# Kernel optimization log

Hardware: AMD Instinct MI355X
Metric: run time of the kernel (lower is better)

The kernel has to match this reference:

```python
import jax, jax.numpy as jnp
import numpy as np

N_QUBITS = 10
EMBED_DIM = 512
FFN_DIM = 2048
DIM = 2 ** N_QUBITS


def _apply_rx(state, theta, wire):
    # state: (N, 2^n) complex64; theta: scalar or (N,)
    N = state.shape[0]
    hi = 2 ** wire                      # dims before the wire axis (wire 0 = MSB)
    lo = 2 ** (N_QUBITS - 1 - wire)
    s = state.reshape(N, hi, 2, lo)
    th = jnp.asarray(theta, jnp.float32).reshape(-1, 1, 1)  # (N,1,1) or (1,1,1)
    c = jnp.cos(th / 2).astype(jnp.complex64)
    ms = (-1j * jnp.sin(th / 2)).astype(jnp.complex64)
    s0, s1 = s[:, :, 0, :], s[:, :, 1, :]
    out = jnp.stack([c * s0 + ms * s1, ms * s0 + c * s1], axis=2)
    return out.reshape(N, DIM)


def _apply_cnot(state, ctrl, tgt):
    N = state.shape[0]
    s = state.reshape((N,) + (2,) * N_QUBITS)
    s0 = jax.lax.index_in_dim(s, 0, axis=ctrl + 1, keepdims=True)
    s1 = jax.lax.index_in_dim(s, 1, axis=ctrl + 1, keepdims=True)
    s1 = jnp.flip(s1, axis=tgt + 1)  # X on target where control == 1
    return jnp.concatenate([s0, s1], axis=ctrl + 1).reshape(N, DIM)


def _pauliz_signs():
    idx = np.arange(DIM)
    bits = (idx[:, None] >> (N_QUBITS - 1 - np.arange(N_QUBITS))[None, :]) & 1
    return jnp.asarray(1.0 - 2.0 * bits, jnp.float32)  # (2^n, n)


def _quantum_layer(tokens, rx_params):
    # tokens: (N, embed_dim); uses first n_qubits features as encoder angles
    N = tokens.shape[0]
    state = jnp.zeros((N, DIM), jnp.complex64).at[:, 0].set(1.0)
    for w in range(N_QUBITS):                    # encoder: RX(x_w) on wire w
        state = _apply_rx(state, tokens[:, w], w)
    for w in range(N_QUBITS):                    # trainable RX per wire
        state = _apply_rx(state, rx_params[w], w)
    for w in range(N_QUBITS - 1):                # CNOT chain
        state = _apply_cnot(state, w, w + 1)
    state = _apply_cnot(state, N_QUBITS - 1, 0)  # wrap-around CNOT
    probs = state.real ** 2 + state.imag ** 2    # (N, 2^n)
    return probs @ _pauliz_signs()               # (N, n_qubits) <Z_w>


def setup_inputs() -> dict:
    key = jax.random.key(0)
    ks = jax.random.split(key, 6)
    x = jax.random.normal(ks[0], (16, 1024, EMBED_DIM), jnp.float32)
    rx_params = jax.random.normal(ks[1], (N_QUBITS,), jnp.float32)
    lim1 = 1.0 / np.sqrt(N_QUBITS)
    w1 = jax.random.uniform(ks[2], (FFN_DIM, N_QUBITS), jnp.float32, -lim1, lim1)
    b1 = jax.random.uniform(ks[3], (FFN_DIM,), jnp.float32, -lim1, lim1)
    lim2 = 1.0 / np.sqrt(FFN_DIM)
    w2 = jax.random.uniform(ks[4], (EMBED_DIM, FFN_DIM), jnp.float32, -lim2, lim2)
    b2 = jax.random.uniform(ks[5], (EMBED_DIM,), jnp.float32, -lim2, lim2)
    return {"x": x, "rx_params": rx_params, "w1": w1, "b1": b1, "w2": w2, "b2": b2}


def reference(x, rx_params, w1, b1, w2, b2):
    B, S, _ = x.shape
    q_out = _quantum_layer(x.reshape(B * S, EMBED_DIM), rx_params)
    q_out = q_out.reshape(B, S, N_QUBITS)
    h = jax.nn.relu(q_out @ w1.T + b1)           # dropout is identity in eval
    return h @ w2.T + b2
```

## Files before the change

### kernel.cpp

```cpp
#include <hip/hip_runtime.h>
#include <hip/hip_bf16.h>
#include <math.h>


typedef __attribute__((ext_vector_type(8))) short short8;
typedef __attribute__((ext_vector_type(8))) unsigned short ushort8;
typedef __attribute__((ext_vector_type(4))) float fx4;

constexpr int EDIM = 512;
constexpr int FDIM = 2048;
constexpr int NQ   = 10;
constexpr int BK   = 64;
constexpr int NCH  = FDIM / BK;

__device__ __forceinline__ ushort f2bf(float f) {
    union { float f; unsigned u; } v; v.f = f;
    unsigned u = v.u + 0x7FFFu + ((v.u >> 16) & 1u);
    return (ushort)(u >> 16);
}
__device__ __forceinline__ unsigned bits2(__hip_bfloat162 h) {
    union { __hip_bfloat162 h; unsigned u; } v; v.h = h; return v.u;
}
__device__ __forceinline__ void gload_lds16(const void* g, void* l) {
    __builtin_amdgcn_global_load_lds(
        (const __attribute__((address_space(1))) void*)g,
        (__attribute__((address_space(3))) void*)l, 16, 0, 0);
}

__global__ void prep(const float* __restrict__ w2, ushort* __restrict__ w2b) {
    int gid = blockIdx.x * blockDim.x + threadIdx.x;
    int np  = gridDim.x * blockDim.x;
    for (int i = gid; i < EDIM * FDIM / 4; i += np) {
        float4 v = ((const float4*)w2)[i];
        ushort4 o; o.x = f2bf(v.x); o.y = f2bf(v.y); o.z = f2bf(v.z); o.w = f2bf(v.w);
        ((ushort4*)w2b)[i] = o;
    }
}

__global__ __launch_bounds__(256, 2) void gemm1(
    const float* __restrict__ x, const float* __restrict__ rx,
    const float* __restrict__ w1, const float* __restrict__ b1,
    ushort* __restrict__ h, int m_base)
{
    __shared__ float qs[32][NQ];
    const int tid = threadIdx.x;
    const int m0  = m_base + blockIdx.x * 32;

    if (tid < 32) {
        const float* xr = x + (size_t)(m0 + tid) * EDIM;
        float c[NQ], q[NQ];
        #pragma unroll
        for (int w = 0; w < NQ; ++w) c[w] = cosf(xr[w] + rx[w]);
        float p0 = c[1];
        #pragma unroll
        for (int w = 2; w < NQ; ++w) p0 *= c[w];
        q[0] = p0;
        float p = c[0];
        #pragma unroll
        for (int w = 1; w < NQ; ++w) { p *= c[w]; q[w] = p; }
        #pragma unroll
        for (int w = 0; w < NQ; ++w) qs[tid][w] = q[w];
    }
    __syncthreads();

    float wv[80];
    {
        const float4* wp = (const float4*)(w1 + (size_t)tid * 80);
        #pragma unroll
        for (int u = 0; u < 20; ++u) ((float4*)wv)[u] = wp[u];
    }
    float bv[8];
    {
        float4 a = *(const float4*)(b1 + tid * 8);
        float4 b = *(const float4*)(b1 + tid * 8 + 4);
        bv[0]=a.x; bv[1]=a.y; bv[2]=a.z; bv[3]=a.w;
        bv[4]=b.x; bv[5]=b.y; bv[6]=b.z; bv[7]=b.w;
    }
    ushort* hrow = h + (size_t)m0 * FDIM + tid * 8;

    for (int m = 0; m < 32; ++m) {
        float qv[NQ];
        #pragma unroll
        for (int w = 0; w < NQ; ++w) qv[w] = qs[m][w];
        float a[8];
        #pragma unroll
        for (int r = 0; r < 8; ++r) a[r] = bv[r];
        #pragma unroll
        for (int w = 0; w < NQ; ++w)
            #pragma unroll
            for (int r = 0; r < 8; ++r)
                a[r] = fmaf(qv[w], wv[r * 10 + w], a[r]);
        ushort8 o;
        #pragma unroll
        for (int r = 0; r < 4; ++r) {
            unsigned p = bits2(__float22bfloat162_rn(
                make_float2(fmaxf(a[2*r], 0.f), fmaxf(a[2*r+1], 0.f))));
            o[2*r]   = (ushort)(p & 0xFFFFu);
            o[2*r+1] = (ushort)(p >> 16);
        }
        *(ushort8*)(hrow + (size_t)m * FDIM) = o;
    }
}

__global__ __launch_bounds__(256, 2) void gemm2(
    const ushort* __restrict__ h,
    const ushort* __restrict__ w2b,
    const float* __restrict__ b2,
    float* __restrict__ out, int m_base)
{
    __shared__ ushort As[128 * BK];
    __shared__ ushort Bs[128 * BK];

    const int tid  = threadIdx.x;
    const int bm   = blockIdx.x;
    const int bn   = blockIdx.y;
    const int m0   = m_base + bm * 128, n0 = bn * 128;
    const int wave = tid >> 6, lane = tid & 63;
    const int quad = lane >> 4, l16 = lane & 15;
    const int wm   = wave >> 1, wn = wave & 1;

    const int srow0 = tid >> 3;
    const int sbs   = tid & 7;
    const ushort* gA[4]; const ushort* gB[4];
    #pragma unroll
    for (int u = 0; u < 4; ++u) {
        int row = u * 32 + srow0;
        int bl  = sbs ^ (row & 7);
        gA[u] = h   + (size_t)(m0 + row) * FDIM + bl * 8;
        gB[u] = w2b + (size_t)(n0 + row) * FDIM + bl * 8;
    }
    const int ldst = wave * 512;

    const int swz = l16 & 7;
    int aro[4], bro[4];
    #pragma unroll
    for (int t = 0; t < 4; ++t) {
        aro[t] = (wm * 64 + t * 16 + l16) * BK;
        bro[t] = (wn * 64 + t * 16 + l16) * BK;
    }

    fx4 acc[4][4];
    #pragma unroll
    for (int a = 0; a < 4; ++a)
        #pragma unroll
        for (int b = 0; b < 4; ++b) acc[a][b] = fx4{0.f, 0.f, 0.f, 0.f};

    for (int i = 0; i < NCH; ++i) {
        #pragma unroll
        for (int u = 0; u < 4; ++u) {
            gload_lds16(gA[u], &As[u * 2048 + ldst]);
            gload_lds16(gB[u], &Bs[u * 2048 + ldst]);
            gA[u] += BK; gB[u] += BK;
        }
        __syncthreads();

        short8 af[4][2], bf[4][2];
        #pragma unroll
        for (int t = 0; t < 4; ++t)
            #pragma unroll
            for (int hf = 0; hf < 2; ++hf) {
                const int blk = (hf * 4 + quad) ^ swz;
                af[t][hf] = *(const short8*)&As[aro[t] + blk * 8];
                bf[t][hf] = *(const short8*)&Bs[bro[t] + blk * 8];
            }

        #pragma unroll
        for (int hf = 0; hf < 2; ++hf)
            #pragma unroll
            for (int mt = 0; mt < 4; ++mt)
                #pragma unroll
                for (int nt = 0; nt < 4; ++nt)
                    acc[mt][nt] = __builtin_amdgcn_mfma_f32_16x16x32_bf16(
                        af[mt][hf], bf[nt][hf], acc[mt][nt], 0, 0, 0);
        __syncthreads();
    }

    float bb[4];
    #pragma unroll
    for (int nt = 0; nt < 4; ++nt) bb[nt] = b2[n0 + wn * 64 + nt * 16 + l16];
    #pragma unroll
    for (int mt = 0; mt < 4; ++mt) {
        const int mbase = m0 + wm * 64 + mt * 16 + quad * 4;
        #pragma unroll
        for (int nt = 0; nt < 4; ++nt) {
            const int n = n0 + wn * 64 + nt * 16 + l16;
            #pragma unroll
            for (int r = 0; r < 4; ++r)
                out[(size_t)(mbase + r) * EDIM + n] = acc[mt][nt][r] + bb[nt];
        }
    }
}

extern "C" void kernel_launch(void* const* d_in, const int* in_sizes, int n_in,
                              void* d_out, int out_size, void* d_ws, size_t ws_size,
                              hipStream_t stream) {
    const float* x  = (const float*)d_in[0];
    const float* rx = (const float*)d_in[1];
    const float* w1 = (const float*)d_in[2];
    const float* b1 = (const float*)d_in[3];
    const float* w2 = (const float*)d_in[4];
    const float* b2 = (const float*)d_in[5];
    float* out = (float*)d_out;

    const int M = in_sizes[0] / EDIM;

    const size_t w2bytes = (size_t)EDIM * FDIM * 2;
    ushort* w2b = (ushort*)d_ws;
    ushort* h   = (ushort*)((char*)d_ws + w2bytes);

    int Ms = M;
    {
        size_t avail = (ws_size > w2bytes) ? ws_size - w2bytes : 0;
        int cap = (int)(avail / ((size_t)FDIM * 2));
        cap &= ~127;
        if (cap < 128) cap = 128;
        if (Ms > cap) Ms = cap;
    }

    hipLaunchKernelGGL(prep, dim3(256), dim3(256), 0, stream, w2, w2b);

    for (int mb = 0; mb < M; mb += Ms) {
        int cur = (M - mb < Ms) ? (M - mb) : Ms;
        hipLaunchKernelGGL(gemm1, dim3(cur / 32), dim3(256), 0, stream,
                           x, rx, w1, b1, h, mb);
        hipLaunchKernelGGL(gemm2, dim3(cur / 128, 4), dim3(256), 0, stream,
                           h, w2b, b2, out, mb);
    }
}
```

Baseline: 140.4 us.

## Fuse quantum layer, FFN1 and FFN2 into one double-buffered MFMA kernel

Replaces the prep, gemm1 and gemm2 kernels with a single fused kernel. Each block computes the quantum expectations and recomputes its 128x64 slice of the hidden activations on the fly for every K chunk. It also converts fp32 w2 to bf16 in registers while staging it into double-buffered LDS, with a 128x256 tile and 512 threads. This removes the global round-trip of the 16Kx2048 bf16 hidden tensor and the separate weight-conversion pass. In exchange, each block redoes the w1 FMAs (the hidden tile is recomputed by both N-blocks), and the loads move from async global_load_lds to synchronous register-staged stores.

```diff
diff --git a/kernel.cpp b/kernel.cpp
--- a/kernel.cpp
+++ b/kernel.cpp
@@ -4,133 +4,93 @@
 
 
 typedef __attribute__((ext_vector_type(8))) short short8;
-typedef __attribute__((ext_vector_type(8))) unsigned short ushort8;
 typedef __attribute__((ext_vector_type(4))) float fx4;
 
 constexpr int EDIM = 512;
 constexpr int FDIM = 2048;
 constexpr int NQ   = 10;
+constexpr int BM   = 128;
+constexpr int BN   = 256;
 constexpr int BK   = 64;
 constexpr int NCH  = FDIM / BK;
 
-__device__ __forceinline__ ushort f2bf(float f) {
-    union { float f; unsigned u; } v; v.f = f;
-    unsigned u = v.u + 0x7FFFu + ((v.u >> 16) & 1u);
-    return (ushort)(u >> 16);
-}
 __device__ __forceinline__ unsigned bits2(__hip_bfloat162 h) {
     union { __hip_bfloat162 h; unsigned u; } v; v.h = h; return v.u;
 }
-__device__ __forceinline__ void gload_lds16(const void* g, void* l) {
-    __builtin_amdgcn_global_load_lds(
-        (const __attribute__((address_space(1))) void*)g,
-        (__attribute__((address_space(3))) void*)l, 16, 0, 0);
-}
-
-__global__ void prep(const float* __restrict__ w2, ushort* __restrict__ w2b) {
-    int gid = blockIdx.x * blockDim.x + threadIdx.x;
-    int np  = gridDim.x * blockDim.x;
-    for (int i = gid; i < EDIM * FDIM / 4; i += np) {
-        float4 v = ((const float4*)w2)[i];
-        ushort4 o; o.x = f2bf(v.x); o.y = f2bf(v.y); o.z = f2bf(v.z); o.w = f2bf(v.w);
-        ((ushort4*)w2b)[i] = o;
-    }
-}
-
-__global__ __launch_bounds__(256, 2) void gemm1(
+
+__device__ __forceinline__ void hcomp(
+    int k1, int fg, const float* __restrict__ w1, const float* __restrict__ b1,
+    const float* q0, const float* q1, float* hv0, float* hv1)
+{
+    const float* w1p = w1 + (size_t)(k1 + fg * 8) * NQ;
+    float b1v[8];
+    *(float4*)(b1v)     = *(const float4*)(b1 + k1 + fg * 8);
+    *(float4*)(b1v + 4) = *(const float4*)(b1 + k1 + fg * 8 + 4);
+    #pragma unroll
+    for (int g = 0; g < 2; ++g) {
+        float wv[40];
+        #pragma unroll
+        for (int u = 0; u < 10; ++u)
+            ((float4*)wv)[u] = ((const float4*)(w1p + g * 40))[u];
+        #pragma unroll
+        for (int j = 0; j < 4; ++j) {
+            float s0 = b1v[g * 4 + j], s1 = s0;
+            #pragma unroll
+            for (int w = 0; w < NQ; ++w) {
+                s0 = fmaf(q0[w], wv[j * 10 + w], s0);
+                s1 = fmaf(q1[w], wv[j * 10 + w], s1);
+            }
+            hv0[g * 4 + j] = s0; hv1[g * 4 + j] = s1;
+        }
+    }
+}
+
+__global__ __launch_bounds__(512, 2) void fused(
     const float* __restrict__ x, const float* __restrict__ rx,
     const float* __restrict__ w1, const float* __restrict__ b1,
-    ushort* __restrict__ h, int m_base)
+    const float* __restrict__ w2, const float* __restrict__ b2,
+    float* __restrict__ out)
 {
-    __shared__ float qs[32][NQ];
+    __shared__ __align__(16) ushort As[2][BM * BK];
+    __shared__ __align__(16) ushort Bs[2][BN * BK];
+    __shared__ float qs[BM][NQ];
+
     const int tid = threadIdx.x;
-    const int m0  = m_base + blockIdx.x * 32;
-
-    if (tid < 32) {
+    const int m0  = blockIdx.x * BM;
+    const int n0  = blockIdx.y * BN;
+
+    if (tid < BM) {
         const float* xr = x + (size_t)(m0 + tid) * EDIM;
-        float c[NQ], q[NQ];
-        #pragma unroll
-        for (int w = 0; w < NQ; ++w) c[w] = cosf(xr[w] + rx[w]);
+        float4 xa = *(const float4*)xr;
+        float4 xb = *(const float4*)(xr + 4);
+        float2 xc = *(const float2*)(xr + 8);
+        float xv[NQ] = {xa.x, xa.y, xa.z, xa.w, xb.x, xb.y, xb.z, xb.w, xc.x, xc.y};
+        float c[NQ];
+        #pragma unroll
+        for (int w = 0; w < NQ; ++w) c[w] = cosf(xv[w] + rx[w]);
         float p0 = c[1];
         #pragma unroll
         for (int w = 2; w < NQ; ++w) p0 *= c[w];
-        q[0] = p0;
+        qs[tid][0] = p0;
         float p = c[0];
         #pragma unroll
-        for (int w = 1; w < NQ; ++w) { p *= c[w]; q[w] = p; }
-        #pragma unroll
-        for (int w = 0; w < NQ; ++w) qs[tid][w] = q[w];
+        for (int w = 1; w < NQ; ++w) { p *= c[w]; qs[tid][w] = p; }
     }
     __syncthreads();
 
-    float wv[80];
-    {
-        const float4* wp = (const float4*)(w1 + (size_t)tid * 80);
-        #pragma unroll
-        for (int u = 0; u < 20; ++u) ((float4*)wv)[u] = wp[u];
-    }
-    float bv[8];
-    {
-        float4 a = *(const float4*)(b1 + tid * 8);
-        float4 b = *(const float4*)(b1 + tid * 8 + 4);
-        bv[0]=a.x; bv[1]=a.y; bv[2]=a.z; bv[3]=a.w;
-        bv[4]=b.x; bv[5]=b.y; bv[6]=b.z; bv[7]=b.w;
-    }
-    ushort* hrow = h + (size_t)m0 * FDIM + tid * 8;
-
-    for (int m = 0; m < 32; ++m) {
-        float qv[NQ];
-        #pragma unroll
-        for (int w = 0; w < NQ; ++w) qv[w] = qs[m][w];
-        float a[8];
-        #pragma unroll
-        for (int r = 0; r < 8; ++r) a[r] = bv[r];
-        #pragma unroll
-        for (int w = 0; w < NQ; ++w)
-            #pragma unroll
-            for (int r = 0; r < 8; ++r)
-                a[r] = fmaf(qv[w], wv[r * 10 + w], a[r]);
-        ushort8 o;
-        #pragma unroll
-        for (int r = 0; r < 4; ++r) {
-            unsigned p = bits2(__float22bfloat162_rn(
-                make_float2(fmaxf(a[2*r], 0.f), fmaxf(a[2*r+1], 0.f))));
-            o[2*r]   = (ushort)(p & 0xFFFFu);
-            o[2*r+1] = (ushort)(p >> 16);
-        }
-        *(ushort8*)(hrow + (size_t)m * FDIM) = o;
-    }
-}
-
-__global__ __launch_bounds__(256, 2) void gemm2(
-    const ushort* __restrict__ h,
-    const ushort* __restrict__ w2b,
-    const float* __restrict__ b2,
-    float* __restrict__ out, int m_base)
-{
-    __shared__ ushort As[128 * BK];
-    __shared__ ushort Bs[128 * BK];
-
-    const int tid  = threadIdx.x;
-    const int bm   = blockIdx.x;
-    const int bn   = blockIdx.y;
-    const int m0   = m_base + bm * 128, n0 = bn * 128;
+    const int fg = tid & 7;
+    const int mg = tid >> 3;
+    float q0[NQ], q1[NQ];
+    #pragma unroll
+    for (int w = 0; w < NQ; ++w) { q0[w] = qs[2 * mg][w]; q1[w] = qs[2 * mg + 1][w]; }
+
+    const int brow = tid >> 1;
+    const int kh   = tid & 1;
+    const float* w2base = w2 + (size_t)(n0 + brow) * FDIM + kh * 32;
+
     const int wave = tid >> 6, lane = tid & 63;
     const int quad = lane >> 4, l16 = lane & 15;
-    const int wm   = wave >> 1, wn = wave & 1;
-
-    const int srow0 = tid >> 3;
-    const int sbs   = tid & 7;
-    const ushort* gA[4]; const ushort* gB[4];
-    #pragma unroll
-    for (int u = 0; u < 4; ++u) {
-        int row = u * 32 + srow0;
-        int bl  = sbs ^ (row & 7);
-        gA[u] = h   + (size_t)(m0 + row) * FDIM + bl * 8;
-        gB[u] = w2b + (size_t)(n0 + row) * FDIM + bl * 8;
-    }
-    const int ldst = wave * 512;
-
+    const int wm = wave >> 2, wn = wave & 3;
     const int swz = l16 & 7;
     int aro[4], bro[4];
     #pragma unroll
@@ -145,34 +105,114 @@
         #pragma unroll
         for (int b = 0; b < 4; ++b) acc[a][b] = fx4{0.f, 0.f, 0.f, 0.f};
 
-    for (int i = 0; i < NCH; ++i) {
-        #pragma unroll
-        for (int u = 0; u < 4; ++u) {
-            gload_lds16(gA[u], &As[u * 2048 + ldst]);
-            gload_lds16(gB[u], &Bs[u * 2048 + ldst]);
-            gA[u] += BK; gB[u] += BK;
-        }
-        __syncthreads();
-
-        short8 af[4][2], bf[4][2];
-        #pragma unroll
-        for (int t = 0; t < 4; ++t)
-            #pragma unroll
-            for (int hf = 0; hf < 2; ++hf) {
-                const int blk = (hf * 4 + quad) ^ swz;
-                af[t][hf] = *(const short8*)&As[aro[t] + blk * 8];
-                bf[t][hf] = *(const short8*)&Bs[bro[t] + blk * 8];
-            }
-
-        #pragma unroll
-        for (int hf = 0; hf < 2; ++hf)
+    float bqv[32];
+    float hv0[8], hv1[8];
+    #pragma unroll
+    for (int u = 0; u < 8; ++u) ((float4*)bqv)[u] = ((const float4*)w2base)[u];
+    hcomp(0, fg, w1, b1, q0, q1, hv0, hv1);
+    {
+        #pragma unroll
+        for (int g = 0; g < 4; ++g) {
+            short8 o;
+            #pragma unroll
+            for (int p = 0; p < 4; ++p) {
+                unsigned u = bits2(__float22bfloat162_rn(
+                    make_float2(bqv[g * 8 + 2 * p], bqv[g * 8 + 2 * p + 1])));
+                o[2 * p] = (short)(u & 0xFFFFu); o[2 * p + 1] = (short)(u >> 16);
+            }
+            const int blk = (kh * 4 + g) ^ (brow & 7);
+            *(short8*)&Bs[0][brow * BK + blk * 8] = o;
+        }
+        #pragma unroll
+        for (int r2 = 0; r2 < 2; ++r2) {
+            const int row = 2 * mg + r2;
+            const float* hv = r2 ? hv1 : hv0;
+            short8 o;
+            #pragma unroll
+            for (int p = 0; p < 4; ++p) {
+                unsigned u = bits2(__float22bfloat162_rn(
+                    make_float2(fmaxf(hv[2 * p], 0.f), fmaxf(hv[2 * p + 1], 0.f))));
+                o[2 * p] = (short)(u & 0xFFFFu); o[2 * p + 1] = (short)(u >> 16);
+            }
+            const int blk = fg ^ (row & 7);
+            *(short8*)&As[0][row * BK + blk * 8] = o;
+        }
+    }
+    __syncthreads();
+
+    for (int i = 0; i < NCH - 1; ++i) {
+        const int cur = i & 1, nxt = cur ^ 1;
+
+        #pragma unroll
+        for (int u = 0; u < 8; ++u)
+            ((float4*)bqv)[u] = ((const float4*)(w2base + (size_t)(i + 1) * BK))[u];
+
+        #pragma unroll
+        for (int hf = 0; hf < 2; ++hf) {
+            const int blk = ((hf * 4 + quad) ^ swz) * 8;
+            short8 af[4], bfq[4];
+            #pragma unroll
+            for (int t = 0; t < 4; ++t) {
+                af[t]  = *(const short8*)&As[cur][aro[t] + blk];
+                bfq[t] = *(const short8*)&Bs[cur][bro[t] + blk];
+            }
             #pragma unroll
             for (int mt = 0; mt < 4; ++mt)
                 #pragma unroll
                 for (int nt = 0; nt < 4; ++nt)
                     acc[mt][nt] = __builtin_amdgcn_mfma_f32_16x16x32_bf16(
-                        af[mt][hf], bf[nt][hf], acc[mt][nt], 0, 0, 0);
+                        af[mt], bfq[nt], acc[mt][nt], 0, 0, 0);
+        }
+
+        hcomp((i + 1) * BK, fg, w1, b1, q0, q1, hv0, hv1);
+
+        #pragma unroll
+        for (int g = 0; g < 4; ++g) {
+            short8 o;
+            #pragma unroll
+            for (int p = 0; p < 4; ++p) {
+                unsigned u = bits2(__float22bfloat162_rn(
+                    make_float2(bqv[g * 8 + 2 * p], bqv[g * 8 + 2 * p + 1])));
+                o[2 * p] = (short)(u & 0xFFFFu); o[2 * p + 1] = (short)(u >> 16);
+            }
+            const int blk = (kh * 4 + g) ^ (brow & 7);
+            *(short8*)&Bs[nxt][brow * BK + blk * 8] = o;
+        }
+        #pragma unroll
+        for (int r2 = 0; r2 < 2; ++r2) {
+            const int row = 2 * mg + r2;
+            const float* hv = r2 ? hv1 : hv0;
+            short8 o;
+            #pragma unroll
+            for (int p = 0; p < 4; ++p) {
+                unsigned u = bits2(__float22bfloat162_rn(
+                    make_float2(fmaxf(hv[2 * p], 0.f), fmaxf(hv[2 * p + 1], 0.f))));
+                o[2 * p] = (short)(u & 0xFFFFu); o[2 * p + 1] = (short)(u >> 16);
+            }
+            const int blk = fg ^ (row & 7);
+            *(short8*)&As[nxt][row * BK + blk * 8] = o;
+        }
         __syncthreads();
+    }
+
+    {
+        const int cur = (NCH - 1) & 1;
+        #pragma unroll
+        for (int hf = 0; hf < 2; ++hf) {
+            const int blk = ((hf * 4 + quad) ^ swz) * 8;
+            short8 af[4], bfq[4];
+            #pragma unroll
+            for (int t = 0; t < 4; ++t) {
+                af[t]  = *(const short8*)&As[cur][aro[t] + blk];
+                bfq[t] = *(const short8*)&Bs[cur][bro[t] + blk];
+            }
+            #pragma unroll
+            for (int mt = 0; mt < 4; ++mt)
+                #pragma unroll
+                for (int nt = 0; nt < 4; ++nt)
+                    acc[mt][nt] = __builtin_amdgcn_mfma_f32_16x16x32_bf16(
+                        af[mt], bfq[nt], acc[mt][nt], 0, 0, 0);
+        }
     }
 
     float bb[4];
@@ -200,30 +240,11 @@
     const float* b1 = (const float*)d_in[3];
     const float* w2 = (const float*)d_in[4];
     const float* b2 = (const float*)d_in[5];
-    float* out = (float*)d_out;
 
     const int M = in_sizes[0] / EDIM;
 
-    const size_t w2bytes = (size_t)EDIM * FDIM * 2;
-    ushort* w2b = (ushort*)d_ws;
-    ushort* h   = (ushort*)((char*)d_ws + w2bytes);
-
-    int Ms = M;
-    {
-        size_t avail = (ws_size > w2bytes) ? ws_size - w2bytes : 0;
-        int cap = (int)(avail / ((size_t)FDIM * 2));
-        cap &= ~127;
-        if (cap < 128) cap = 128;
-        if (Ms > cap) Ms = cap;
-    }
-
-    hipLaunchKernelGGL(prep, dim3(256), dim3(256), 0, stream, w2, w2b);
-
-    for (int mb = 0; mb < M; mb += Ms) {
-        int cur = (M - mb < Ms) ? (M - mb) : Ms;
-        hipLaunchKernelGGL(gemm1, dim3(cur / 32), dim3(256), 0, stream,
-                           x, rx, w1, b1, h, mb);
-        hipLaunchKernelGGL(gemm2, dim3(cur / 128, 4), dim3(256), 0, stream,
-                           h, w2b, b2, out, mb);
-    }
-}
+    (void)d_ws; (void)ws_size; (void)n_in; (void)out_size;
+
+    hipLaunchKernelGGL(fused, dim3(M / BM, EDIM / BN), dim3(512), 0, stream,
+                       x, rx, w1, b1, w2, b2, (float*)d_out);
+}
```

New measurement: 240.7 us. 71.4% more time.

## Double-buffer gemm2 LDS tiles with 256x128 blocks and interleaved MFMA phases

Applied to the files above, without the earlier changes.

Rewrites the second GEMM to use 512-thread blocks with 256x128 output tiles and double-buffered LDS. Global-to-LDS loads for the next K tile are issued between MFMA quadrant phases, using explicit vmcnt waits, barriers and setprio to overlap memory with compute. This replaces the load-sync-compute-sync loop that exposed load latency each iteration. It increases LDS use to 96KB per block, which limits occupancy, and relies on hand-placed waitcnts being correct.

```diff
diff --git a/kernel.cpp b/kernel.cpp
--- a/kernel.cpp
+++ b/kernel.cpp
@@ -11,7 +11,11 @@
 constexpr int FDIM = 2048;
 constexpr int NQ   = 10;
 constexpr int BK   = 64;
-constexpr int NCH  = FDIM / BK;
+constexpr int BM2  = 256;
+constexpr int BN2  = 128;
+constexpr int NT2  = FDIM / BK;
+constexpr int ABUF = BM2 * BK;
+constexpr int BBUF = BN2 * BK;
 
 __device__ __forceinline__ ushort f2bf(float f) {
     union { float f; unsigned u; } v; v.f = f;
@@ -26,6 +30,12 @@
         (const __attribute__((address_space(1))) void*)g,
         (__attribute__((address_space(3))) void*)l, 16, 0, 0);
 }
+
+#define SBAR()   __builtin_amdgcn_s_barrier()
+#define LGKM0()  asm volatile("s_waitcnt lgkmcnt(0)" ::: "memory")
+#define SCHED0() __builtin_amdgcn_sched_barrier(0)
+#define VMCNT6() asm volatile("s_waitcnt vmcnt(6)" ::: "memory")
+#define VMCNT0() asm volatile("s_waitcnt vmcnt(0)" ::: "memory")
 
 __global__ void prep(const float* __restrict__ w2, ushort* __restrict__ w2b) {
     int gid = blockIdx.x * blockDim.x + threadIdx.x;
@@ -102,36 +112,33 @@
     }
 }
 
-__global__ __launch_bounds__(256, 2) void gemm2(
+__global__ __launch_bounds__(512, 2) void gemm2(
     const ushort* __restrict__ h,
     const ushort* __restrict__ w2b,
     const float* __restrict__ b2,
     float* __restrict__ out, int m_base)
 {
-    __shared__ ushort As[128 * BK];
-    __shared__ ushort Bs[128 * BK];
+    __shared__ __align__(16) ushort As[2 * ABUF];
+    __shared__ __align__(16) ushort Bs[2 * BBUF];
 
     const int tid  = threadIdx.x;
-    const int bm   = blockIdx.x;
-    const int bn   = blockIdx.y;
-    const int m0   = m_base + bm * 128, n0 = bn * 128;
+    const int m0   = m_base + blockIdx.x * BM2;
+    const int n0   = blockIdx.y * BN2;
     const int wave = tid >> 6, lane = tid & 63;
     const int quad = lane >> 4, l16 = lane & 15;
     const int wm   = wave >> 1, wn = wave & 1;
-
-    const int srow0 = tid >> 3;
-    const int sbs   = tid & 7;
-    const ushort* gA[4]; const ushort* gB[4];
-    #pragma unroll
-    for (int u = 0; u < 4; ++u) {
-        int row = u * 32 + srow0;
-        int bl  = sbs ^ (row & 7);
-        gA[u] = h   + (size_t)(m0 + row) * FDIM + bl * 8;
-        gB[u] = w2b + (size_t)(n0 + row) * FDIM + bl * 8;
-    }
-    const int ldst = wave * 512;
-
-    const int swz = l16 & 7;
+    const int swz  = l16 & 7;
+
+    const int srow = tid >> 3;
+    const int bl   = (tid & 7) ^ (srow & 7);
+    const ushort* pA[4]; const ushort* pB[2];
+    #pragma unroll
+    for (int u = 0; u < 4; ++u)
+        pA[u] = h + (size_t)(m0 + u * 64 + srow) * FDIM + bl * 8;
+    #pragma unroll
+    for (int u = 0; u < 2; ++u)
+        pB[u] = w2b + (size_t)(n0 + u * 64 + srow) * FDIM + bl * 8;
+
     int aro[4], bro[4];
     #pragma unroll
     for (int t = 0; t < 4; ++t) {
@@ -145,35 +152,79 @@
         #pragma unroll
         for (int b = 0; b < 4; ++b) acc[a][b] = fx4{0.f, 0.f, 0.f, 0.f};
 
-    for (int i = 0; i < NCH; ++i) {
-        #pragma unroll
-        for (int u = 0; u < 4; ++u) {
-            gload_lds16(gA[u], &As[u * 2048 + ldst]);
-            gload_lds16(gB[u], &Bs[u * 2048 + ldst]);
-            gA[u] += BK; gB[u] += BK;
-        }
-        __syncthreads();
-
-        short8 af[4][2], bf[4][2];
-        #pragma unroll
-        for (int t = 0; t < 4; ++t)
-            #pragma unroll
-            for (int hf = 0; hf < 2; ++hf) {
-                const int blk = (hf * 4 + quad) ^ swz;
-                af[t][hf] = *(const short8*)&As[aro[t] + blk * 8];
-                bf[t][hf] = *(const short8*)&Bs[bro[t] + blk * 8];
-            }
-
-        #pragma unroll
-        for (int hf = 0; hf < 2; ++hf)
-            #pragma unroll
-            for (int mt = 0; mt < 4; ++mt)
-                #pragma unroll
-                for (int nt = 0; nt < 4; ++nt)
-                    acc[mt][nt] = __builtin_amdgcn_mfma_f32_16x16x32_bf16(
-                        af[mt][hf], bf[nt][hf], acc[mt][nt], 0, 0, 0);
-        __syncthreads();
-    }
+#define RDA(Ab, PAIR, fr) do { \
+    _Pragma("unroll") for (int m_ = 0; m_ < 2; ++m_) \
+    _Pragma("unroll") for (int hf = 0; hf < 2; ++hf) \
+        fr[m_][hf] = *(const short8*)&(Ab)[aro[(PAIR)*2+m_] + (((hf*4+quad)^swz)<<3)]; \
+} while(0)
+#define RDB(Bb, PAIR, fr) do { \
+    _Pragma("unroll") for (int n_ = 0; n_ < 2; ++n_) \
+    _Pragma("unroll") for (int hf = 0; hf < 2; ++hf) \
+        fr[n_][hf] = *(const short8*)&(Bb)[bro[(PAIR)*2+n_] + (((hf*4+quad)^swz)<<3)]; \
+} while(0)
+#define MMQ(Af, Bf, MO, NO) do { \
+    _Pragma("unroll") for (int hf = 0; hf < 2; ++hf) \
+    _Pragma("unroll") for (int m_ = 0; m_ < 2; ++m_) \
+    _Pragma("unroll") for (int n_ = 0; n_ < 2; ++n_) \
+        acc[(MO)+m_][(NO)+n_] = __builtin_amdgcn_mfma_f32_16x16x32_bf16( \
+            Af[m_][hf], Bf[n_][hf], acc[(MO)+m_][(NO)+n_], 0, 0, 0); \
+} while(0)
+
+    #pragma unroll
+    for (int u = 0; u < 4; ++u) { gload_lds16(pA[u], As + u * 4096 + wave * 512); pA[u] += BK; }
+    #pragma unroll
+    for (int u = 0; u < 2; ++u) { gload_lds16(pB[u], Bs + u * 4096 + wave * 512); pB[u] += BK; }
+    #pragma unroll
+    for (int u = 0; u < 4; ++u) { gload_lds16(pA[u], As + ABUF + u * 4096 + wave * 512); pA[u] += BK; }
+    #pragma unroll
+    for (int u = 0; u < 2; ++u) { gload_lds16(pB[u], Bs + BBUF + u * 4096 + wave * 512); pB[u] += BK; }
+    VMCNT6();
+    SBAR();
+
+#define KTILE(T, MODE) do { \
+    const ushort* Ab = As + ((T) & 1) * ABUF; \
+    const ushort* Bb = Bs + ((T) & 1) * BBUF; \
+    ushort* Aw = As + ((T) & 1) * ABUF; \
+    ushort* Bw = Bs + ((T) & 1) * BBUF; \
+    short8 a0[2][2], a1[2][2], b0[2][2], b1[2][2]; \
+     \
+    RDA(Ab, 0, a0); RDB(Bb, 0, b0); \
+    SBAR(); LGKM0(); SCHED0(); \
+    __builtin_amdgcn_s_setprio(1); MMQ(a0, b0, 0, 0); __builtin_amdgcn_s_setprio(0); \
+    SBAR(); \
+     \
+    RDB(Bb, 1, b1); \
+    SBAR(); LGKM0(); SCHED0(); \
+    __builtin_amdgcn_s_setprio(1); MMQ(a0, b1, 0, 2); __builtin_amdgcn_s_setprio(0); \
+    SBAR(); \
+     \
+    RDA(Ab, 1, a1); \
+    if ((MODE) == 0) { \
+        _Pragma("unroll") for (int u = 0; u < 2; ++u) { \
+            gload_lds16(pB[u], Bw + u * 4096 + wave * 512); pB[u] += BK; } \
+    } \
+    SBAR(); LGKM0(); SCHED0(); \
+    __builtin_amdgcn_s_setprio(1); MMQ(a1, b1, 2, 2); __builtin_amdgcn_s_setprio(0); \
+    SBAR(); \
+     \
+    if ((MODE) == 0) { \
+        _Pragma("unroll") for (int u = 0; u < 4; ++u) { \
+            gload_lds16(pA[u], Aw + u * 4096 + wave * 512); pA[u] += BK; } \
+        VMCNT6(); \
+    } else if ((MODE) == 1) { VMCNT0(); } \
+    SBAR(); \
+    __builtin_amdgcn_s_setprio(1); MMQ(a1, b0, 2, 0); __builtin_amdgcn_s_setprio(0); \
+    SBAR(); \
+} while(0)
+
+    for (int t = 0; t < NT2 - 2; ++t) KTILE(t, 0);
+    KTILE(NT2 - 2, 1);
+    KTILE(NT2 - 1, 2);
+
+#undef KTILE
+#undef MMQ
+#undef RDA
+#undef RDB
 
     float bb[4];
     #pragma unroll
@@ -212,8 +263,8 @@
     {
         size_t avail = (ws_size > w2bytes) ? ws_size - w2bytes : 0;
         int cap = (int)(avail / ((size_t)FDIM * 2));
-        cap &= ~127;
-        if (cap < 128) cap = 128;
+        cap &= ~255;
+        if (cap < 256) cap = 256;
         if (Ms > cap) Ms = cap;
     }
 
@@ -223,7 +274,7 @@
         int cur = (M - mb < Ms) ? (M - mb) : Ms;
         hipLaunchKernelGGL(gemm1, dim3(cur / 32), dim3(256), 0, stream,
                            x, rx, w1, b1, h, mb);
-        hipLaunchKernelGGL(gemm2, dim3(cur / 128, 4), dim3(256), 0, stream,
+        hipLaunchKernelGGL(gemm2, dim3(cur / BM2, EDIM / BN2), dim3(512), 0, stream,
                            h, w2b, b2, out, mb);
     }
 }
```

Result: slower. 146.9 us (+4.6%).

## Triple-buffer gemm2 LDS loads and enlarge tile to 256x128 with 8 waves

Applied to the files above, without the earlier changes.

Rewrites the second GEMM main loop as a three-stage software pipeline. Async global-to-LDS loads for a future K chunk are issued before computing on the current chunk, and only vmcnt-counted waits plus a single barrier are used per iteration. The block tile grows to 256x128 with 512 threads, which improves reuse of the B operand. MFMA sections are wrapped in raised wave priority. The cost is about 147KB of LDS per block, which allows only one block per CU, and the grid is halved to 256 blocks.

```diff
diff --git a/kernel.cpp b/kernel.cpp
--- a/kernel.cpp
+++ b/kernel.cpp
@@ -11,7 +11,11 @@
 constexpr int FDIM = 2048;
 constexpr int NQ   = 10;
 constexpr int BK   = 64;
-constexpr int NCH  = FDIM / BK;
+constexpr int BM2  = 256;
+constexpr int BN2  = 128;
+constexpr int NT2  = FDIM / BK;
+constexpr int ABUF = BM2 * BK;
+constexpr int BBUF = BN2 * BK;
 
 __device__ __forceinline__ ushort f2bf(float f) {
     union { float f; unsigned u; } v; v.f = f;
@@ -26,6 +30,11 @@
         (const __attribute__((address_space(1))) void*)g,
         (__attribute__((address_space(3))) void*)l, 16, 0, 0);
 }
+
+#define SBAR()   __builtin_amdgcn_s_barrier()
+#define FENCE()  asm volatile("" ::: "memory")
+#define VMCNT6() asm volatile("s_waitcnt vmcnt(6)" ::: "memory")
+#define VMCNT0() asm volatile("s_waitcnt vmcnt(0)" ::: "memory")
 
 __global__ void prep(const float* __restrict__ w2, ushort* __restrict__ w2b) {
     int gid = blockIdx.x * blockDim.x + threadIdx.x;
@@ -102,36 +111,33 @@
     }
 }
 
-__global__ __launch_bounds__(256, 2) void gemm2(
+__global__ __launch_bounds__(512, 2) void gemm2(
     const ushort* __restrict__ h,
     const ushort* __restrict__ w2b,
     const float* __restrict__ b2,
     float* __restrict__ out, int m_base)
 {
-    __shared__ ushort As[128 * BK];
-    __shared__ ushort Bs[128 * BK];
+    __shared__ __align__(16) ushort As[3 * ABUF];
+    __shared__ __align__(16) ushort Bs[3 * BBUF];
 
     const int tid  = threadIdx.x;
-    const int bm   = blockIdx.x;
-    const int bn   = blockIdx.y;
-    const int m0   = m_base + bm * 128, n0 = bn * 128;
+    const int m0   = m_base + blockIdx.x * BM2;
+    const int n0   = blockIdx.y * BN2;
     const int wave = tid >> 6, lane = tid & 63;
     const int quad = lane >> 4, l16 = lane & 15;
     const int wm   = wave >> 1, wn = wave & 1;
-
-    const int srow0 = tid >> 3;
-    const int sbs   = tid & 7;
-    const ushort* gA[4]; const ushort* gB[4];
-    #pragma unroll
-    for (int u = 0; u < 4; ++u) {
-        int row = u * 32 + srow0;
-        int bl  = sbs ^ (row & 7);
-        gA[u] = h   + (size_t)(m0 + row) * FDIM + bl * 8;
-        gB[u] = w2b + (size_t)(n0 + row) * FDIM + bl * 8;
-    }
-    const int ldst = wave * 512;
-
-    const int swz = l16 & 7;
+    const int swz  = l16 & 7;
+
+    const int srow = tid >> 3;
+    const int bl   = (tid & 7) ^ (srow & 7);
+    const ushort* pA[4]; const ushort* pB[2];
+    #pragma unroll
+    for (int u = 0; u < 4; ++u)
+        pA[u] = h + (size_t)(m0 + u * 64 + srow) * FDIM + bl * 8;
+    #pragma unroll
+    for (int u = 0; u < 2; ++u)
+        pB[u] = w2b + (size_t)(n0 + u * 64 + srow) * FDIM + bl * 8;
+
     int aro[4], bro[4];
     #pragma unroll
     for (int t = 0; t < 4; ++t) {
@@ -145,35 +151,70 @@
         #pragma unroll
         for (int b = 0; b < 4; ++b) acc[a][b] = fx4{0.f, 0.f, 0.f, 0.f};
 
-    for (int i = 0; i < NCH; ++i) {
-        #pragma unroll
-        for (int u = 0; u < 4; ++u) {
-            gload_lds16(gA[u], &As[u * 2048 + ldst]);
-            gload_lds16(gB[u], &Bs[u * 2048 + ldst]);
-            gA[u] += BK; gB[u] += BK;
-        }
-        __syncthreads();
-
+#define STAGE_A(dst) do { _Pragma("unroll") \
+    for (int u = 0; u < 4; ++u) { gload_lds16(pA[u], (dst) + u * 4096 + wave * 512); pA[u] += BK; } } while(0)
+#define STAGE_B(dst) do { _Pragma("unroll") \
+    for (int u = 0; u < 2; ++u) { gload_lds16(pB[u], (dst) + u * 4096 + wave * 512); pB[u] += BK; } } while(0)
+#define RDFRAGS(Ab, Bb, af, bf) do { _Pragma("unroll") \
+    for (int t = 0; t < 4; ++t) _Pragma("unroll") \
+    for (int hf = 0; hf < 2; ++hf) { \
+        const int blk = (((hf * 4 + quad) ^ swz) << 3); \
+        af[t][hf] = *(const short8*)&(Ab)[aro[t] + blk]; \
+        bf[t][hf] = *(const short8*)&(Bb)[bro[t] + blk]; \
+    } } while(0)
+#define MMALL(af, bf) do { _Pragma("unroll") \
+    for (int hf = 0; hf < 2; ++hf) _Pragma("unroll") \
+    for (int mt = 0; mt < 4; ++mt) _Pragma("unroll") \
+    for (int nt = 0; nt < 4; ++nt) \
+        acc[mt][nt] = __builtin_amdgcn_mfma_f32_16x16x32_bf16( \
+            af[mt][hf], bf[nt][hf], acc[mt][nt], 0, 0, 0); } while(0)
+
+    STAGE_A(As); STAGE_B(Bs);
+    STAGE_A(As + ABUF); STAGE_B(Bs + BBUF);
+    VMCNT6();
+    SBAR(); FENCE();
+
+    int cur = 0, stg = 2;
+    for (int t = 0; t < NT2 - 2; ++t) {
+        ushort* Aw = As + stg * ABUF;
+        ushort* Bw = Bs + stg * BBUF;
+        STAGE_A(Aw); STAGE_B(Bw);
+
+        const ushort* Ab = As + cur * ABUF;
+        const ushort* Bb = Bs + cur * BBUF;
         short8 af[4][2], bf[4][2];
-        #pragma unroll
-        for (int t = 0; t < 4; ++t)
-            #pragma unroll
-            for (int hf = 0; hf < 2; ++hf) {
-                const int blk = (hf * 4 + quad) ^ swz;
-                af[t][hf] = *(const short8*)&As[aro[t] + blk * 8];
-                bf[t][hf] = *(const short8*)&Bs[bro[t] + blk * 8];
-            }
-
-        #pragma unroll
-        for (int hf = 0; hf < 2; ++hf)
-            #pragma unroll
-            for (int mt = 0; mt < 4; ++mt)
-                #pragma unroll
-                for (int nt = 0; nt < 4; ++nt)
-                    acc[mt][nt] = __builtin_amdgcn_mfma_f32_16x16x32_bf16(
-                        af[mt][hf], bf[nt][hf], acc[mt][nt], 0, 0, 0);
-        __syncthreads();
-    }
+        RDFRAGS(Ab, Bb, af, bf);
+        __builtin_amdgcn_s_setprio(1);
+        MMALL(af, bf);
+        __builtin_amdgcn_s_setprio(0);
+
+        VMCNT6();
+        SBAR(); FENCE();
+        cur = (cur == 2) ? 0 : cur + 1;
+        stg = (stg == 2) ? 0 : stg + 1;
+    }
+
+    {
+        short8 af[4][2], bf[4][2];
+        RDFRAGS(As, Bs, af, bf);
+        __builtin_amdgcn_s_setprio(1);
+        MMALL(af, bf);
+        __builtin_amdgcn_s_setprio(0);
+        VMCNT0();
+        SBAR(); FENCE();
+    }
+    {
+        short8 af[4][2], bf[4][2];
+        RDFRAGS(As + ABUF, Bs + BBUF, af, bf);
+        __builtin_amdgcn_s_setprio(1);
+        MMALL(af, bf);
+        __builtin_amdgcn_s_setprio(0);
+    }
+
+#undef MMALL
+#undef RDFRAGS
+#undef STAGE_A
+#undef STAGE_B
 
     float bb[4];
     #pragma unroll
@@ -212,8 +253,8 @@
     {
         size_t avail = (ws_size > w2bytes) ? ws_size - w2bytes : 0;
         int cap = (int)(avail / ((size_t)FDIM * 2));
-        cap &= ~127;
-        if (cap < 128) cap = 128;
+        cap &= ~255;
+        if (cap < 256) cap = 256;
         if (Ms > cap) Ms = cap;
     }
 
@@ -223,7 +264,7 @@
         int cur = (M - mb < Ms) ? (M - mb) : Ms;
         hipLaunchKernelGGL(gemm1, dim3(cur / 32), dim3(256), 0, stream,
                            x, rx, w1, b1, h, mb);
-        hipLaunchKernelGGL(gemm2, dim3(cur / 128, 4), dim3(256), 0, stream,
+        hipLaunchKernelGGL(gemm2, dim3(cur / BM2, EDIM / BN2), dim3(512), 0, stream,
                            h, w2b, b2, out, mb);
     }
 }
```

After: 148.9 us. 6.1% more time.
